# Kernel tuning notes

Hardware: AMD Instinct MI355X
Metric: run time of the kernel (lower is better)

Reference implementation:

```python
import jax, jax.numpy as jnp
from jax import lax
import numpy as np

# dims (match init_kwargs config)
B, L, D = 32, 512, 32          # batch, seq_len, input_dim
H = 256                         # hidden_dim
E = 8                           # num_experts
PLEN, O = 96, 32                # pred_len, output_dim
LAT = 256                       # flow latent_dim
PD, NPROT = 64, 16              # prototype_dim, num_prototypes


def setup_inputs() -> dict:
    key = jax.random.key(0)
    ks = iter(jax.random.split(key, 40))
    def n(shape, scale=0.02):
        return (jax.random.normal(next(ks), shape, jnp.float32) * scale)
    inp = {
        'x': jax.random.normal(next(ks), (B, L, D), jnp.float32),
        # prototypes + projector (metric gating / diversity)
        'prototypes': n((NPROT, PD), 0.5),
        'Wp': n((PD, PD)), 'bp': jnp.zeros((PD,), jnp.float32),
        # expert_feature_extractor: Linear(7D->H), ReLU, Linear(H->PD), LayerNorm(PD)
        'Wf1': n((7 * D, H)), 'bf1': jnp.zeros((H,), jnp.float32),
        'Wf2': n((H, PD)), 'bf2': jnp.zeros((PD,), jnp.float32),
        'ln_g': jnp.ones((PD,), jnp.float32), 'ln_b': jnp.zeros((PD,), jnp.float32),
        # flow encoder (latent mapping of flattened window) + gating head
        'W1': n((L * D, H)), 'b1': jnp.zeros((H,), jnp.float32),
        'W2': n((H, LAT)), 'b2': jnp.zeros((LAT,), jnp.float32),
        'Wg': n((LAT, E)), 'bg': jnp.zeros((E,), jnp.float32),
        'log_temp': jnp.zeros((), jnp.float32),
        # stacked FFT+Mamba expert params (leading axis = expert)
        'Win': n((E, D, H)), 'b_in': jnp.zeros((E, H), jnp.float32),
        'Wfft': n((E, H, H)), 'b_fft': jnp.zeros((E, H), jnp.float32),
        'a_logit': n((E, H), 1.0),
        'Whead': n((E, H, PLEN * O)), 'b_head': jnp.zeros((E, PLEN * O), jnp.float32),
    }
    return inp


def _expert_features(x, Wf1, bf1, Wf2, bf2, ln_g, ln_b):
    # faithful to compute_expert_features: 7 per-channel stats -> MLP -> LayerNorm
    Lf = jnp.float32(x.shape[1])
    x_mean = x.mean(axis=1)
    x_std = x.std(axis=1, ddof=1)             # torch unbiased std
    x_min = x.min(axis=1)
    x_max = x.max(axis=1)
    x_diff_mean = jnp.diff(x, axis=1).mean(axis=1)
    x_trend = (x[:, -1, :] - x[:, 0, :]) / Lf
    x_fft_mag = jnp.abs(jnp.fft.fft(x, axis=1)).mean(axis=1)
    cf = jnp.concatenate([x_mean, x_std, x_min, x_max, x_diff_mean, x_trend, x_fft_mag], axis=1)
    h = jax.nn.relu(cf @ Wf1 + bf1)
    ef = h @ Wf2 + bf2
    mu = ef.mean(axis=-1, keepdims=True)
    var = ef.var(axis=-1, keepdims=True)
    return (ef - mu) / jnp.sqrt(var + 1e-5) * ln_g + ln_b


def reference(x, prototypes, Wp, bp, Wf1, bf1, Wf2, bf2, ln_g, ln_b,
              W1, b1, W2, b2, Wg, bg, log_temp,
              Win, b_in, Wfft, b_fft, a_logit, Whead, b_head):
    b, l, d = x.shape
    # --- metric-based gating ---
    ef = _expert_features(x, Wf1, bf1, Wf2, bf2, ln_g, ln_b)           # [B,PD]
    latent = jax.nn.relu(x.reshape(b, -1) @ W1 + b1) @ W2 + b2          # flow latent [B,LAT]
    lg = latent @ Wg + bg                                               # [B,E]
    proj = ef @ Wp + bp                                                 # prototype_projector
    d2 = ((proj[:, None, :] - prototypes[None, :, :]) ** 2).sum(-1)     # [B,NPROT]
    d2_per_expert = d2.reshape(b, E, NPROT // E).min(axis=-1)           # min dist to each expert's prototypes
    temp = jnp.clip(jnp.exp(log_temp), 0.1, 10.0)
    w = jax.nn.softmax((lg - d2_per_expert) / temp, axis=-1)            # [B,E]

    # --- FFT + Mamba-style experts (vmapped over stacked expert params) ---
    def expert(Win_e, b_in_e, Wfft_e, b_fft_e, a_logit_e, Whead_e, b_head_e):
        h = jnp.einsum('bld,dh->blh', x, Win_e) + b_in_e                # [B,L,H]
        f = jnp.einsum('blh,hk->blk', jnp.abs(jnp.fft.fft(h, axis=1)), Wfft_e) + b_fft_e
        u = jax.nn.relu(h + f)
        a = jax.nn.sigmoid(a_logit_e)                                   # per-channel decay
        def step(s, ut):
            s = a * s + (1.0 - a) * ut
            return s, None
        s_last, _ = lax.scan(step, jnp.zeros((b, H), x.dtype), jnp.swapaxes(u, 0, 1))
        return (s_last @ Whead_e + b_head_e).reshape(b, PLEN, O)

    outs = jax.vmap(expert)(Win, b_in, Wfft, b_fft, a_logit, Whead, b_head)  # [E,B,PLEN,O]
    y = jnp.einsum('be,ebpo->bpo', w, outs)
    return y
```

## Files before the change

kernel.cpp:

```cpp
#include <hip/hip_runtime.h>
#include <hip/hip_bf16.h>


typedef __hip_bfloat16 bf16;
typedef unsigned short u16;
typedef __attribute__((ext_vector_type(8))) short s8v;
typedef __attribute__((ext_vector_type(4))) float f4v;

#define MFMA_BF16(a,b,c) __builtin_amdgcn_mfma_f32_16x16x32_bf16(a,b,c,0,0,0)

#if __has_builtin(__builtin_amdgcn_sqrtf)
#define FSQRT(x) __builtin_amdgcn_sqrtf(x)
#else
#define FSQRT(x) sqrtf(x)
#endif
#if __has_builtin(__builtin_amdgcn_exp2f)
#define FEXP2(x) __builtin_amdgcn_exp2f(x)
#else
#define FEXP2(x) exp2f(x)
#endif
#if __has_builtin(__builtin_amdgcn_logf)
#define FLOG2(x) __builtin_amdgcn_logf(x)
#else
#define FLOG2(x) log2f(x)
#endif

#define GWF1 0
#define GW2  57344
#define GWF2 122880
#define GWP  139264
#define GPROT 143360
#define GWG  144384

__device__ __forceinline__ float bf2f(u16 u){
  union{ unsigned u32; float f; } w; w.u32 = ((unsigned)u) << 16; return w.f;
}
__device__ __forceinline__ u16 f2bf(float f){
  bf16 h = __float2bfloat16(f);
  union{ bf16 b; u16 u; } w; w.b = h; return w.u;
}
__device__ __forceinline__ u16 f2bf_fast(float f){
  union{ float f; unsigned u; } v; v.f = f;
  unsigned r = v.u + 0x7FFFu + ((v.u >> 16) & 1u);
  return (u16)(r >> 16);
}
__device__ __forceinline__ float ldg_(const void* p, long long i, bool bf){
  float r;
  if(bf) r = bf2f(((const u16*)p)[i]);
  else   r = ((const float*)p)[i];
  return r;
}
__device__ __forceinline__ bool bfflag(const void* ln_g){
  return ((const u16*)ln_g)[0] == 0x3F80;
}

__global__ __launch_bounds__(256) void ks1(const void* __restrict__ ln_g,
    const void* __restrict__ x,
    const void* __restrict__ Win, const void* __restrict__ Wfft,
    const void* __restrict__ W1, const void* __restrict__ Whead,
    const void* __restrict__ Wf1, const void* __restrict__ W2,
    const void* __restrict__ Wf2, const void* __restrict__ Wp,
    const void* __restrict__ prot, const void* __restrict__ Wg,
    u16* __restrict__ xbf,
    u16* __restrict__ WinTg, u16* __restrict__ WfftTg,
    u16* __restrict__ W1Tg, u16* __restrict__ WheadTg,
    u16* __restrict__ gw,
    u16* __restrict__ Xr, u16* __restrict__ Xi, float* __restrict__ cf){
  const bool bf = bfflag(ln_g);
  __shared__ float xs[512], re[512], im[512];
  __shared__ float twr[256], twi[256];
  __shared__ float r0s[4], r1s[4], r2s[4], r3s[4];
  __shared__ u16 tile[64][72];
  int BX = blockIdx.x, t = threadIdx.x;

  if(BX < 1024){
    int b = BX >> 5, d = BX & 31;
    {
      float rev = -(float)t * (1.f/512.f);
#if __has_builtin(__builtin_amdgcn_cosf) && __has_builtin(__builtin_amdgcn_sinf)
      twr[t] = __builtin_amdgcn_cosf(rev);
      twi[t] = __builtin_amdgcn_sinf(rev);
#else
      float ang = rev * 6.283185307179586f;
      twr[t] = cosf(ang); twi[t] = sinf(ang);
#endif
    }
    for(int i=t;i<512;i+=256){
      float v = ldg_(x, (long long)(b*512+i)*32 + d, bf);
      xs[i] = v;
      re[__brev((unsigned)i) >> 23] = v;
      im[i] = 0.f;
    }
    __syncthreads();
    float s=0.f, s2=0.f, mn=3.0e38f, mx=-3.0e38f;
    for(int i=t;i<512;i+=256){ float v=xs[i]; s+=v; s2+=v*v; mn=fminf(mn,v); mx=fmaxf(mx,v); }
    #pragma unroll
    for(int o=32;o>0;o>>=1){
      s  += __shfl_down(s,o);  s2 += __shfl_down(s2,o);
      mn = fminf(mn,__shfl_down(mn,o)); mx = fmaxf(mx,__shfl_down(mx,o));
    }
    int wv = t>>6, ln = t&63;
    if(ln==0){ r0s[wv]=s; r1s[wv]=s2; r2s[wv]=mn; r3s[wv]=mx; }
    __syncthreads();
    if(t==0){
      float S =r0s[0]+r0s[1]+r0s[2]+r0s[3];
      float S2=r1s[0]+r1s[1]+r1s[2]+r1s[3];
      float MN=fminf(fminf(r2s[0],r2s[1]),fminf(r2s[2],r2s[3]));
      float MX=fmaxf(fmaxf(r3s[0],r3s[1]),fmaxf(r3s[2],r3s[3]));
      float mean = S*(1.f/512.f);
      float var  = (S2 - S*S*(1.f/512.f))*(1.f/511.f);
      float* c = cf + b*224;
      c[d]      = mean;
      c[32+d]   = sqrtf(fmaxf(var,0.f));
      c[64+d]   = MN;
      c[96+d]   = MX;
      float dv = xs[511]-xs[0];
      c[128+d]  = dv*(1.f/511.f);
      c[160+d]  = dv*(1.f/512.f);
    }
    for(int st=1; st<=9; ++st){
      __syncthreads();
      int m = 1<<st, half = m>>1;
      int grp = t >> (st-1);
      int k   = t & (half-1);
      int i1 = grp*m + k, i2 = i1 + half;
      int ti_ = k << (9-st);
      float cs = twr[ti_], sn = twi[ti_];
      float ar=re[i1], ai=im[i1], br=re[i2], bi=im[i2];
      float tr = cs*br - sn*bi;
      float ti = cs*bi + sn*br;
      re[i1]=ar+tr; im[i1]=ai+ti;
      re[i2]=ar-tr; im[i2]=ai-ti;
    }
    __syncthreads();
    float ms=0.f;
    for(int i=t;i<512;i+=256){
      float rr=re[i], ii=im[i];
      long long o = (long long)(b*512+i)*32 + d;
      Xr[o]=f2bf(rr); Xi[o]=f2bf(ii);
      ms += FSQRT(rr*rr+ii*ii);
    }
    #pragma unroll
    for(int o=32;o>0;o>>=1) ms += __shfl_down(ms,o);
    if(ln==0) r0s[wv]=ms;
    __syncthreads();
    if(t==0) cf[b*224 + 192 + d] = (r0s[0]+r0s[1]+r0s[2]+r0s[3])*(1.f/512.f);
    return;
  }
  if(BX < 4111){
    int bx = BX - 1024;
    if(bx < 256){
      int i = bx*256 + t;
      int e = i >> 13, r = i & 8191;
      int c = r >> 5, d = r & 31;
      WinTg[i] = f2bf(ldg_(Win, (long long)e*8192 + d*256 + c, bf));
      return;
    }
    if(bx < 384){
      int idx = bx - 256;
      int e = idx >> 4, tl = idx & 15, kb = tl >> 2, cb = tl & 3;
      if(bf){
        for(int q=0;q<16;q++){
          int G = q*256 + t; int ki = G >> 6, ci = G & 63;
          tile[ci][ki] = ((const u16*)Wfft)[(long long)e*65536 + (long long)(kb*64+ki)*256 + cb*64+ci];
        }
      } else {
        for(int q=0;q<16;q++){
          int G = q*256 + t; int ki = G >> 6, ci = G & 63;
          tile[ci][ki] = f2bf(((const float*)Wfft)[(long long)e*65536 + (long long)(kb*64+ki)*256 + cb*64+ci]);
        }
      }
      __syncthreads();
      for(int q=0;q<16;q++){
        int G = q*256 + t; int ci = G >> 6, ki = G & 63;
        WfftTg[(long long)e*65536 + (long long)(cb*64+ci)*256 + kb*64+ki] = tile[ci][ki];
      }
      return;
    }
    if(bx < 1408){
      int idx = bx - 384;
      int kb = idx & 255, nb = idx >> 8;
      if(bf){
        for(int q=0;q<16;q++){
          int G = q*256 + t; int ki = G >> 6, ni = G & 63;
          tile[ni][ki] = ((const u16*)W1)[(long long)(kb*64+ki)*256 + nb*64+ni];
        }
      } else {
        for(int q=0;q<16;q++){
          int G = q*256 + t; int ki = G >> 6, ni = G & 63;
          tile[ni][ki] = f2bf(((const float*)W1)[(long long)(kb*64+ki)*256 + nb*64+ni]);
        }
      }
      __syncthreads();
      for(int q=0;q<16;q++){
        int G = q*256 + t; int ni = G >> 6, ki = G & 63;
        W1Tg[(long long)(nb*64+ni)*16384 + kb*64+ki] = tile[ni][ki];
      }
      return;
    }
    if(bx < 2944){
      int idx = bx - 1408;
      int e = idx / 192, rem = idx % 192;
      int kb = rem / 48, nb = rem % 48;
      if(bf){
        for(int q=0;q<16;q++){
          int G = q*256 + t; int ki = G >> 6, ni = G & 63;
          tile[ni][ki] = ((const u16*)Whead)[(long long)e*786432 + (long long)(kb*64+ki)*3072 + nb*64+ni];
        }
      } else {
        for(int q=0;q<16;q++){
          int G = q*256 + t; int ki = G >> 6, ni = G & 63;
          tile[ni][ki] = f2bf(((const float*)Whead)[(long long)e*786432 + (long long)(kb*64+ki)*3072 + nb*64+ni]);
        }
      }
      __syncthreads();
      for(int q=0;q<16;q++){
        int G = q*256 + t; int ni = G >> 6, ki = G & 63;
        WheadTg[(long long)e*786432 + (long long)(nb*64+ni)*256 + kb*64+ki] = tile[ni][ki];
      }
      return;
    }
    {
      int c = bx - 2944;
      const void* src; int dstbase, blkoff;
      if(c < 56)      { src=Wf1;  dstbase=GWF1;  blkoff=c; }
      else if(c <120) { src=W2;   dstbase=GW2;   blkoff=c-56; }
      else if(c <136) { src=Wf2;  dstbase=GWF2;  blkoff=c-120; }
      else if(c <140) { src=Wp;   dstbase=GWP;   blkoff=c-136; }
      else if(c <141) { src=prot; dstbase=GPROT; blkoff=0; }
      else            { src=Wg;   dstbase=GWG;   blkoff=c-141; }
      int i = blkoff*1024 + t*4;
      if(bf){
        ushort4 v = *(const ushort4*)((const u16*)src + i);
        *(ushort4*)(gw + dstbase + i) = v;
      } else {
        float4 f = *(const float4*)((const float*)src + i);
        ushort4 v; v.x=f2bf(f.x); v.y=f2bf(f.y); v.z=f2bf(f.z); v.w=f2bf(f.w);
        *(ushort4*)(gw + dstbase + i) = v;
      }
    }
    return;
  }
  {
    int i = ((BX-4111)*256 + t)*4;
    if(bf){
      ushort4 v = *(const ushort4*)((const u16*)x + i);
      *(ushort4*)(xbf+i) = v;
    } else {
      float4 f = *(const float4*)((const float*)x + i);
      ushort4 v; v.x=f2bf(f.x); v.y=f2bf(f.y); v.z=f2bf(f.z); v.w=f2bf(f.w);
      *(ushort4*)(xbf+i) = v;
    }
  }
}

__global__ __launch_bounds__(256) void ks2(const void* __restrict__ ln_g,
    const u16* __restrict__ xbf, const u16* __restrict__ Xr, const u16* __restrict__ Xi,
    const u16* __restrict__ WinTg, const u16* __restrict__ W1Tg,
    const u16* __restrict__ gw, const float* __restrict__ cf,
    const void* __restrict__ bf1, const void* __restrict__ b_in,
    const void* __restrict__ b_fft, const void* __restrict__ a_logit,
    const void* __restrict__ Win, const void* __restrict__ Wfft,
    float* __restrict__ psum, u16* __restrict__ hmagG,
    float* __restrict__ h1f, float* __restrict__ contrib){
  const bool bf = bfflag(ln_g);
  int BX = blockIdx.x, t = threadIdx.x;
  int w = t >> 6, lane = t & 63, quad = lane >> 4, l15 = lane & 15;
  const f4v zf = (f4v){0.f,0.f,0.f,0.f};
  __shared__ float binS[256];
  __shared__ float cfs[224];
  __shared__ float hm[256];
  __shared__ float xr6[32], xi6[32], x6[32];

  if(BX < 64){
    int kb = BX;
    f4v acc[2][4];
    #pragma unroll
    for(int mt=0;mt<2;mt++)
      #pragma unroll
      for(int nt=0;nt<4;nt++) acc[mt][nt] = zf;
    #pragma unroll
    for(int ks=0;ks<8;ks++){
      long long k = kb*256 + ks*32 + quad*8;
      s8v aF[2], bF[4];
      #pragma unroll
      for(int mt=0;mt<2;mt++)
        aF[mt] = *(const s8v*)(xbf + (long long)(mt*16 + l15)*16384 + k);
      #pragma unroll
      for(int nt=0;nt<4;nt++)
        bF[nt] = *(const s8v*)(W1Tg + (long long)(w*64 + nt*16 + l15)*16384 + k);
      #pragma unroll
      for(int mt=0;mt<2;mt++)
        #pragma unroll
        for(int nt=0;nt<4;nt++)
          acc[mt][nt] = MFMA_BF16(aF[mt], bF[nt], acc[mt][nt]);
    }
    float* po = psum + (long long)kb*8192;
    #pragma unroll
    for(int mt=0;mt<2;mt++)
      #pragma unroll
      for(int nt=0;nt<4;nt++)
        #pragma unroll
        for(int r=0;r<4;r++)
          po[(mt*16 + quad*4 + r)*256 + w*64 + nt*16 + l15] = acc[mt][nt][r];
    return;
  }
  if(BX < 1088){
    int bx = BX - 64;
    int e = bx >> 7, inner = bx & 127;
    int b = inner >> 2, half = (inner >> 1) & 1, kh = inner & 1;
    int row0 = b*512 + half*128;
    binS[t] = ldg_(b_in, e*256+t, bf);
    s8v xrF[2], xiF[2];
    #pragma unroll
    for(int nt=0;nt<2;nt++){
      long long row = row0 + w*32 + nt*16 + l15;
      xrF[nt] = *(const s8v*)(Xr + row*32 + quad*8);
      xiF[nt] = *(const s8v*)(Xi + row*32 + quad*8);
    }
    __syncthreads();
    u16* Ho = hmagG + (long long)((e<<6)|(b<<1)|half)*32768;
    #pragma unroll
    for(int kcl=0;kcl<2;kcl++){
      int k0 = (kh*2+kcl)*64;
      #pragma unroll
      for(int ct=0;ct<4;ct++){
        s8v wfr = *(const s8v*)(WinTg + ((long long)e*256 + k0 + ct*16 + l15)*32 + quad*8);
        #pragma unroll
        for(int nt=0;nt<2;nt++){
          f4v hr = MFMA_BF16(wfr, xrF[nt], zf);
          f4v hi = MFMA_BF16(wfr, xiF[nt], zf);
          int rowg = row0 + w*32 + nt*16 + l15;
          bool bin0 = ((rowg & 511) == 0);
          ushort4 pk;
          int cb4 = k0 + ct*16 + quad*4;
          float h0 = hr[0] + (bin0 ? 512.f*binS[cb4+0] : 0.f);
          float h1 = hr[1] + (bin0 ? 512.f*binS[cb4+1] : 0.f);
          float h2 = hr[2] + (bin0 ? 512.f*binS[cb4+2] : 0.f);
          float h3 = hr[3] + (bin0 ? 512.f*binS[cb4+3] : 0.f);
          pk.x = f2bf_fast(FSQRT(h0*h0 + hi[0]*hi[0]));
          pk.y = f2bf_fast(FSQRT(h1*h1 + hi[1]*hi[1]));
          pk.z = f2bf_fast(FSQRT(h2*h2 + hi[2]*hi[2]));
          pk.w = f2bf_fast(FSQRT(h3*h3 + hi[3]*hi[3]));
          *(ushort4*)&Ho[(w*32 + nt*16 + l15)*256 + cb4] = pk;
        }
      }
    }
    return;
  }
  if(BX < 1120){
    int b = BX - 1088;
    if(t < 224) cfs[t] = cf[(long long)b*224 + t];
    __syncthreads();
    float a1 = ldg_(bf1, t, bf);
    const u16* Wp_ = gw + GWF1 + t;
    #pragma unroll 16
    for(int k=0;k<224;k++) a1 += cfs[k]*bf2f(Wp_[k*256]);
    h1f[b*256+t] = fmaxf(a1, 0.f);
    return;
  }
  {
    int bx = BX - 1120;
    int e = bx >> 5, b = bx & 31, j = t;
    if(j < 32){
      long long o = ((long long)(b*512 + 256))*32 + j;
      xr6[j] = bf2f(Xr[o]);
      xi6[j] = bf2f(Xi[o]);
      x6[j]  = bf2f(xbf[o]);
    }
    __syncthreads();
    float sr=0.f, si=0.f, hx=0.f;
    if(bf){
      const u16* Wn = (const u16*)Win + (long long)e*8192 + j;
      #pragma unroll 8
      for(int d=0; d<32; d++){
        float wv = bf2f(Wn[d*256]);
        sr += xr6[d]*wv; si += xi6[d]*wv; hx += x6[d]*wv;
      }
    } else {
      const float* Wn = (const float*)Win + (long long)e*8192 + j;
      #pragma unroll 8
      for(int d=0; d<32; d++){
        float wv = Wn[d*256];
        sr += xr6[d]*wv; si += xi6[d]*wv; hx += x6[d]*wv;
      }
    }
    hm[j] = FSQRT(sr*sr + si*si);
    __syncthreads();
    float f = 0.f;
    if(bf){
      const u16* Wf = (const u16*)Wfft + (long long)e*65536 + j;
      #pragma unroll 8
      for(int k=0;k<256;k++) f += hm[k]*bf2f(Wf[(long long)k*256]);
    } else {
      const float* Wf = (const float*)Wfft + (long long)e*65536 + j;
      #pragma unroll 8
      for(int k=0;k<256;k++) f += hm[k]*Wf[(long long)k*256];
    }
    float a = 1.f/(1.f+__expf(-ldg_(a_logit, e*256+j, bf)));
    a = fminf(fmaxf(a, 1e-12f), 0.99999988f);
    float l2a = FLOG2(a);
    float u = fmaxf(hx + f + ldg_(b_in,e*256+j,bf) + ldg_(b_fft,e*256+j,bf), 0.f);
    contrib[(e*32+b)*256 + j] = u * FEXP2(l2a * 255.f);
  }
}

__global__ __launch_bounds__(256) void ks3(const void* __restrict__ ln_g,
    const float* __restrict__ psum, const float* __restrict__ h1f,
    const u16* __restrict__ gw,
    const void* __restrict__ b1, const void* __restrict__ bf2,
    const void* __restrict__ ln_b, const void* __restrict__ bp,
    const void* __restrict__ b2, const void* __restrict__ bg,
    const void* __restrict__ log_temp,
    const u16* __restrict__ xbf, const u16* __restrict__ hmagG,
    const u16* __restrict__ WinTg, const u16* __restrict__ WfftTg,
    const void* __restrict__ b_in, const void* __restrict__ b_fft,
    const void* __restrict__ a_logit,
    float* __restrict__ wgt, float* __restrict__ sp){
  const bool bf = bfflag(ln_g);
  int BX = blockIdx.x, t = threadIdx.x;
  __shared__ __align__(16) u16 BsT[128][72];
  __shared__ float biasS[128], l2aS[128], aS[128];
  __shared__ float hsL[256], h1L[256], latL[256], efL[64], prL[64];
  __shared__ float red[4][64];
  __shared__ float d2part[16][16], d2s[16], lgpart[32][8];

  if(BX < 32){
    int b = BX;
    {
      float s0=0.f, s1=0.f, s2=0.f, s3=0.f;
      #pragma unroll
      for(int kb=0;kb<64;kb+=4){
        s0 += psum[(long long)(kb+0)*8192 + b*256 + t];
        s1 += psum[(long long)(kb+1)*8192 + b*256 + t];
        s2 += psum[(long long)(kb+2)*8192 + b*256 + t];
        s3 += psum[(long long)(kb+3)*8192 + b*256 + t];
      }
      hsL[t] = fmaxf((s0+s1)+(s2+s3) + ldg_(b1,t,bf), 0.f);
    }
    h1L[t] = h1f[b*256+t];
    __syncthreads();
    {
      float a = ldg_(b2, t, bf);
      const u16* W2p = gw + GW2 + t;
      #pragma unroll 16
      for(int k=0;k<256;k++) a += hsL[k]*bf2f(W2p[k*256]);
      latL[t] = a;
    }
    {
      int p = t>>6, j = t&63;
      float acc = 0.f;
      const u16* Wf2p = gw + GWF2 + p*64*64 + j;
      #pragma unroll 16
      for(int i=0;i<64;i++) acc += h1L[p*64+i]*bf2f(Wf2p[i*64]);
      red[p][j] = acc;
    }
    __syncthreads();
    if(t < 64){
      float a2 = red[0][t]+red[1][t]+red[2][t]+red[3][t] + ldg_(bf2,t,bf);
      float sm=a2, sq=a2*a2;
      #pragma unroll
      for(int o=32;o>0;o>>=1){ sm += __shfl_xor(sm,o); sq += __shfl_xor(sq,o); }
      float mu  = sm*(1.f/64.f);
      float var = sq*(1.f/64.f) - mu*mu;
      efL[t] = (a2-mu)*rsqrtf(fmaxf(var,0.f)+1e-5f)*ldg_(ln_g,t,bf) + ldg_(ln_b,t,bf);
      float p_acc = ldg_(bp, t, bf);
      const u16* Wpp = gw + GWP + t;
      #pragma unroll 16
      for(int k=0;k<64;k++) p_acc += efL[k]*bf2f(Wpp[k*64]);
      prL[t] = p_acc;
    }
    {
      int part = t>>3, e = t&7;
      float gp = 0.f;
      const u16* Wgp = gw + GWG + e;
      #pragma unroll
      for(int i=0;i<8;i++){
        int k = part*8 + i;
        gp += latL[k]*bf2f(Wgp[k*8]);
      }
      lgpart[part][e] = gp;
    }
    __syncthreads();
    {
      int p = t>>4, q4 = t&15;
      float dd = 0.f;
      #pragma unroll
      for(int i=0;i<4;i++){
        int d = q4*4 + i;
        float df = prL[d] - bf2f(gw[GPROT + p*64 + d]);
        dd += df*df;
      }
      d2part[p][q4] = dd;
    }
    __syncthreads();
    if(t < 16){
      float s = 0.f;
      #pragma unroll
      for(int i=0;i<16;i++) s += d2part[t][i];
      d2s[t] = s;
    }
    __syncthreads();
    if(t < 8){
      float g = ldg_(bg, t, bf);
      #pragma unroll
      for(int p=0;p<32;p++) g += lgpart[p][t];
      float d2pe = fminf(d2s[2*t], d2s[2*t+1]);
      float temp = fminf(fmaxf(__expf(ldg_(log_temp,0,bf)), 0.1f), 10.f);
      float v = (g - d2pe) / temp;
      float m = v;
      m = fmaxf(m, __shfl_xor(m,1));
      m = fmaxf(m, __shfl_xor(m,2));
      m = fmaxf(m, __shfl_xor(m,4));
      float ex = __expf(v-m);
      float sum = ex;
      sum += __shfl_xor(sum,1);
      sum += __shfl_xor(sum,2);
      sum += __shfl_xor(sum,4);
      wgt[b*8+t] = ex/sum;
    }
    return;
  }
  {
    int bx = BX - 32;
    int e = bx >> 7, inner = bx & 127;
    int b = inner >> 2, half = (inner >> 1) & 1, cb = inner & 1;
    int row0 = b*512 + half*128;
    int col0 = cb*128;
    int w = t >> 6, lane = t & 63, quad = lane >> 4, l15 = lane & 15;

    if(t < 128){
      int c = col0 + t;
      biasS[t] = ldg_(b_in, e*256+c, bf) + ldg_(b_fft, e*256+c, bf);
      float a = 1.f/(1.f+__expf(-ldg_(a_logit, e*256+c, bf)));
      a = fminf(fmaxf(a, 1e-12f), 0.99999988f);
      aS[t] = a;
      l2aS[t] = FLOG2(a);
    }
    const u16* Ab = hmagG + (long long)((e<<6)|(b<<1)|half)*32768;
    const f4v zf = (f4v){0.f,0.f,0.f,0.f};
    f4v acc[2][8];
    #pragma unroll
    for(int mt=0;mt<2;mt++)
      #pragma unroll
      for(int nt=0;nt<8;nt++) acc[mt][nt] = zf;

    for(int kc=0;kc<4;kc++){
      int k0 = kc*64;
      __syncthreads();
      #pragma unroll
      for(int q=0;q<4;q++){
        int G = q*256 + t;
        int c = G >> 3, k8 = (G & 7)*8;
        *(s8v*)&BsT[c][k8] = *(const s8v*)(WfftTg + ((long long)e*256 + col0 + c)*256 + k0 + k8);
      }
      __syncthreads();
      #pragma unroll
      for(int ks=0;ks<2;ks++){
        int kb = ks*32 + quad*8;
        s8v aF0 = *(const s8v*)(Ab + (w*32 + l15)*256 + k0 + kb);
        s8v aF1 = *(const s8v*)(Ab + (w*32 + 16 + l15)*256 + k0 + kb);
        #pragma unroll
        for(int nt=0;nt<8;nt++){
          s8v bF = *(const s8v*)&BsT[nt*16 + l15][kb];
          acc[0][nt] = MFMA_BF16(aF0, bF, acc[0][nt]);
          acc[1][nt] = MFMA_BF16(aF1, bF, acc[1][nt]);
        }
      }
    }
    s8v xF[2], xFm[2];
    #pragma unroll
    for(int mt=0;mt<2;mt++){
      long long rowO = (long long)row0 + w*32 + mt*16 + l15;
      xF[mt] = *(const s8v*)(xbf + rowO*32 + quad*8);
      int lin = half*128 + w*32 + mt*16 + l15;
      int lm  = (512 - lin) & 511;
      xFm[mt] = *(const s8v*)(xbf + ((long long)b*512 + lm)*32 + quad*8);
    }
    int l0base = half*128 + w*32 + quad*4;
    float mz = (l0base == 0) ? 0.f : 1.f;
    const f4v zf2 = (f4v){0.f,0.f,0.f,0.f};
    float part[8];
    #pragma unroll
    for(int nt=0;nt<8;nt++){
      s8v wfh = *(const s8v*)(WinTg + ((long long)e*256 + col0 + nt*16 + l15)*32 + quad*8);
      f4v hv0 = MFMA_BF16(xF[0],  wfh, zf2);
      f4v hv1 = MFMA_BF16(xF[1],  wfh, zf2);
      f4v hm0 = MFMA_BF16(xFm[0], wfh, zf2);
      f4v hm1 = MFMA_BF16(xFm[1], wfh, zf2);
      int cl = nt*16 + l15;
      float l2a = l2aS[cl], bias = biasS[cl], av = aS[cl];
      float inv_a = FEXP2(-l2a);
      float cO0 = FEXP2(l2a * (float)(511 - l0base));
      float cO1 = FEXP2(l2a * (float)(495 - l0base));
      float cM0 = FEXP2(l2a * (float)(l0base - 1));
      float cM1 = FEXP2(l2a * (float)(l0base + 15));
      float sum = 0.f;
      #pragma unroll
      for(int r=0;r<4;r++){
        float u0 = fmaxf(acc[0][nt][r] + hv0[r] + bias, 0.f);
        sum += u0 * cO0;
        float u1 = fmaxf(acc[1][nt][r] + hv1[r] + bias, 0.f);
        sum += u1 * cO1;
        float m0 = fmaxf(acc[0][nt][r] + hm0[r] + bias, 0.f);
        float w0 = m0 * cM0;
        if(r == 0) w0 *= mz;
        sum += w0;
        float m1 = fmaxf(acc[1][nt][r] + hm1[r] + bias, 0.f);
        sum += m1 * cM1;
        cO0 *= inv_a; cO1 *= inv_a; cM0 *= av; cM1 *= av;
      }
      part[nt] = sum;
    }
    __syncthreads();
    float (*redS)[132] = (float(*)[132])BsT;
    #pragma unroll
    for(int nt=0;nt<8;nt++)
      redS[w*4 + quad][nt*16 + l15] = part[nt];
    __syncthreads();
    if(t < 128){
      float tot = 0.f;
      #pragma unroll
      for(int i=0;i<16;i++) tot += redS[i][t];
      sp[e*16384 + (b*2 + half)*256 + col0 + t] = tot;
    }
  }
}

__global__ __launch_bounds__(256) void k67(const void* __restrict__ ln_g,
    const float* __restrict__ sp, const float* __restrict__ contrib,
    const float* __restrict__ wgt, const void* __restrict__ a_logit,
    const u16* __restrict__ WheadTg, const void* __restrict__ b_head,
    void* __restrict__ out){
  const bool bf = bfflag(ln_g);
  int nb = blockIdx.x, t = threadIdx.x;
  int w = t >> 6, lane = t & 63, quad = lane >> 4, l15 = lane & 15;
  __shared__ __align__(16) u16 ssS[32][264];
  __shared__ float omaS[2048];
  __shared__ float wgtS[256];

  wgtS[t] = wgt[t];
  #pragma unroll
  for(int q=0;q<8;q++){
    int idx = q*256 + t;
    float a = 1.f/(1.f+__expf(-ldg_(a_logit, idx, bf)));
    a = fminf(fmaxf(a, 1e-12f), 0.99999988f);
    omaS[idx] = 1.f - a;
  }
  const f4v zf = (f4v){0.f,0.f,0.f,0.f};
  f4v acc[2][2];
  #pragma unroll
  for(int mt=0;mt<2;mt++)
    #pragma unroll
    for(int nt=0;nt<2;nt++) acc[mt][nt] = zf;

  for(int e=0;e<8;e++){
    __syncthreads();
    {
      float oma = omaS[e*256 + t];
      const float* sp0 = sp + e*16384 + t;
      const float* cb  = contrib + e*8192 + t;
      #pragma unroll
      for(int q=0;q<32;q++){
        float v = oma*(sp0[q*512] + sp0[q*512+256] + cb[q*256]);
        ssS[q][t] = f2bf(v);
      }
    }
    __syncthreads();
    f4v tmp[2][2];
    #pragma unroll
    for(int mt=0;mt<2;mt++)
      #pragma unroll
      for(int nt=0;nt<2;nt++) tmp[mt][nt] = zf;
    #pragma unroll
    for(int ks=0;ks<8;ks++){
      int k = ks*32 + quad*8;
      s8v aF0 = *(const s8v*)&ssS[l15][k];
      s8v aF1 = *(const s8v*)&ssS[16 + l15][k];
      s8v bF[2];
      #pragma unroll
      for(int nt=0;nt<2;nt++)
        bF[nt] = *(const s8v*)(WheadTg + ((long long)e*3072 + nb*128 + w*32 + nt*16 + l15)*256 + k);
      tmp[0][0] = MFMA_BF16(aF0, bF[0], tmp[0][0]);
      tmp[0][1] = MFMA_BF16(aF0, bF[1], tmp[0][1]);
      tmp[1][0] = MFMA_BF16(aF1, bF[0], tmp[1][0]);
      tmp[1][1] = MFMA_BF16(aF1, bF[1], tmp[1][1]);
    }
    #pragma unroll
    for(int nt=0;nt<2;nt++){
      int col = nb*128 + w*32 + nt*16 + l15;
      float bh = ldg_(b_head, (long long)e*3072 + col, bf);
      #pragma unroll
      for(int mt=0;mt<2;mt++)
        #pragma unroll
        for(int r=0;r<4;r++){
          int b = mt*16 + quad*4 + r;
          acc[mt][nt][r] += wgtS[b*8+e]*(tmp[mt][nt][r] + bh);
        }
    }
  }
  #pragma unroll
  for(int mt=0;mt<2;mt++)
    #pragma unroll
    for(int nt=0;nt<2;nt++){
      int col = nb*128 + w*32 + nt*16 + l15;
      #pragma unroll
      for(int r=0;r<4;r++){
        int b = mt*16 + quad*4 + r;
        long long i = (long long)b*3072 + col;
        if(bf) ((u16*)out)[i] = f2bf(acc[mt][nt][r]);
        else   ((float*)out)[i] = acc[mt][nt][r];
      }
    }
}

extern "C" void kernel_launch(void* const* d_in, const int* in_sizes, int n_in,
                              void* d_out, int out_size, void* d_ws, size_t ws_size,
                              hipStream_t stream){
  const void* x       = d_in[0];
  const void* prot    = d_in[1];
  const void* Wp      = d_in[2];
  const void* bp      = d_in[3];
  const void* Wf1     = d_in[4];
  const void* bf1     = d_in[5];
  const void* Wf2     = d_in[6];
  const void* bf2     = d_in[7];
  const void* ln_g    = d_in[8];
  const void* ln_b    = d_in[9];
  const void* W1      = d_in[10];
  const void* b1      = d_in[11];
  const void* W2      = d_in[12];
  const void* b2      = d_in[13];
  const void* Wg      = d_in[14];
  const void* bg      = d_in[15];
  const void* log_temp= d_in[16];
  const void* Win     = d_in[17];
  const void* b_in    = d_in[18];
  const void* Wfft    = d_in[19];
  const void* b_fft   = d_in[20];
  const void* a_logit = d_in[21];
  const void* Whead   = d_in[22];
  const void* b_head  = d_in[23];

  float* ws      = (float*)d_ws;
  float* cf      = ws;
  float* wgt     = cf + 7168;
  float* sp      = wgt + 256;
  float* h1f     = sp + 131072;
  float* contrib = sp + 262144;
  float* psum    = sp + 262144 + 786432;
  u16*   Xr      = (u16*)(psum + 524288);
  u16*   Xi      = Xr + 524288;
  u16*   xbf     = Xi + 524288;
  u16*   WinTg   = xbf + 524288;
  u16*   WfftTg  = WinTg + 65536;
  u16*   W1Tg    = WfftTg + 524288;
  u16*   WheadTg = W1Tg + 4194304;
  u16*   ssbf    = WheadTg + 6291456;
  u16*   gw      = ssbf + 65536;
  u16*   hmagG   = gw + 146432;

  ks1 <<<dim3(4623), dim3(256), 0, stream>>>(ln_g, x, Win, Wfft, W1, Whead,
                                             Wf1, W2, Wf2, Wp, prot, Wg,
                                             xbf, WinTg, WfftTg, W1Tg, WheadTg, gw,
                                             Xr, Xi, cf);
  ks2 <<<dim3(1376), dim3(256), 0, stream>>>(ln_g, xbf, Xr, Xi, WinTg, W1Tg,
                                             gw, cf, bf1, b_in, b_fft, a_logit,
                                             Win, Wfft,
                                             psum, hmagG, h1f, contrib);
  ks3 <<<dim3(1056), dim3(256), 0, stream>>>(ln_g, psum, h1f, gw,
                                             b1, bf2, ln_b, bp, b2, bg, log_temp,
                                             xbf, hmagG, WinTg, WfftTg,
                                             b_in, b_fft, a_logit,
                                             wgt, sp);
  k67 <<<dim3(24),   dim3(256), 0, stream>>>(ln_g, sp, contrib, wgt, a_logit,
                                             WheadTg, b_head, d_out);
}
```

Before: 224.6 us.

## Split head GEMM across experts into separate grid and add mixing kernel

The final head kernel, which looped over all eight experts inside only 24 blocks, becomes a 24x8 grid. Each block computes one expert's head GEMM and writes its unmixed result to a workspace buffer. A new elementwise kernel then applies the gating weights and biases across experts to produce the output. The FFT stage also stops storing spectrum bins above the Nyquist index, relying on conjugate symmetry of the real-input FFT, and the workspace layout is compacted. The cost is an extra launch and a round trip through global memory for the per-expert results.

```diff
diff --git a/kernel.cpp b/kernel.cpp
--- a/kernel.cpp
+++ b/kernel.cpp
@@ -136,8 +136,10 @@
     float ms=0.f;
     for(int i=t;i<512;i+=256){
       float rr=re[i], ii=im[i];
-      long long o = (long long)(b*512+i)*32 + d;
-      Xr[o]=f2bf(rr); Xi[o]=f2bf(ii);
+      if(i <= 256){
+        long long o = (long long)(b*512+i)*32 + d;
+        Xr[o]=f2bf(rr); Xi[o]=f2bf(ii);
+      }
       ms += FSQRT(rr*rr+ii*ii);
     }
     #pragma unroll
@@ -627,91 +629,76 @@
   }
 }
 
-__global__ __launch_bounds__(256) void k67(const void* __restrict__ ln_g,
+__global__ __launch_bounds__(256) void k6_mfma(const void* __restrict__ ln_g,
     const float* __restrict__ sp, const float* __restrict__ contrib,
-    const float* __restrict__ wgt, const void* __restrict__ a_logit,
-    const u16* __restrict__ WheadTg, const void* __restrict__ b_head,
-    void* __restrict__ out){
+    const void* __restrict__ a_logit,
+    const u16* __restrict__ WheadTg, float* __restrict__ yaccE){
   const bool bf = bfflag(ln_g);
-  int nb = blockIdx.x, t = threadIdx.x;
+  int nb = blockIdx.x, e = blockIdx.y;
+  int t = threadIdx.x;
   int w = t >> 6, lane = t & 63, quad = lane >> 4, l15 = lane & 15;
   __shared__ __align__(16) u16 ssS[32][264];
-  __shared__ float omaS[2048];
-  __shared__ float wgtS[256];
-
-  wgtS[t] = wgt[t];
-  #pragma unroll
-  for(int q=0;q<8;q++){
-    int idx = q*256 + t;
-    float a = 1.f/(1.f+__expf(-ldg_(a_logit, idx, bf)));
+  {
+    float a = 1.f/(1.f+__expf(-ldg_(a_logit, e*256+t, bf)));
     a = fminf(fmaxf(a, 1e-12f), 0.99999988f);
-    omaS[idx] = 1.f - a;
-  }
+    float oma = 1.f - a;
+    const float* sp0 = sp + e*16384 + t;
+    const float* cb  = contrib + e*8192 + t;
+    #pragma unroll
+    for(int q=0;q<32;q++){
+      float v = oma*(sp0[q*512] + sp0[q*512+256] + cb[q*256]);
+      ssS[q][t] = f2bf(v);
+    }
+  }
+  __syncthreads();
   const f4v zf = (f4v){0.f,0.f,0.f,0.f};
   f4v acc[2][2];
   #pragma unroll
   for(int mt=0;mt<2;mt++)
     #pragma unroll
     for(int nt=0;nt<2;nt++) acc[mt][nt] = zf;
-
-  for(int e=0;e<8;e++){
-    __syncthreads();
-    {
-      float oma = omaS[e*256 + t];
-      const float* sp0 = sp + e*16384 + t;
-      const float* cb  = contrib + e*8192 + t;
-      #pragma unroll
-      for(int q=0;q<32;q++){
-        float v = oma*(sp0[q*512] + sp0[q*512+256] + cb[q*256]);
-        ssS[q][t] = f2bf(v);
-      }
-    }
-    __syncthreads();
-    f4v tmp[2][2];
-    #pragma unroll
-    for(int mt=0;mt<2;mt++)
-      #pragma unroll
-      for(int nt=0;nt<2;nt++) tmp[mt][nt] = zf;
-    #pragma unroll
-    for(int ks=0;ks<8;ks++){
-      int k = ks*32 + quad*8;
-      s8v aF0 = *(const s8v*)&ssS[l15][k];
-      s8v aF1 = *(const s8v*)&ssS[16 + l15][k];
-      s8v bF[2];
-      #pragma unroll
-      for(int nt=0;nt<2;nt++)
-        bF[nt] = *(const s8v*)(WheadTg + ((long long)e*3072 + nb*128 + w*32 + nt*16 + l15)*256 + k);
-      tmp[0][0] = MFMA_BF16(aF0, bF[0], tmp[0][0]);
-      tmp[0][1] = MFMA_BF16(aF0, bF[1], tmp[0][1]);
-      tmp[1][0] = MFMA_BF16(aF1, bF[0], tmp[1][0]);
-      tmp[1][1] = MFMA_BF16(aF1, bF[1], tmp[1][1]);
-    }
+  #pragma unroll
+  for(int ks=0;ks<8;ks++){
+    int k = ks*32 + quad*8;
+    s8v aF0 = *(const s8v*)&ssS[l15][k];
+    s8v aF1 = *(const s8v*)&ssS[16 + l15][k];
+    s8v bF[2];
+    #pragma unroll
+    for(int nt=0;nt<2;nt++)
+      bF[nt] = *(const s8v*)(WheadTg + ((long long)e*3072 + nb*128 + w*32 + nt*16 + l15)*256 + k);
+    acc[0][0] = MFMA_BF16(aF0, bF[0], acc[0][0]);
+    acc[0][1] = MFMA_BF16(aF0, bF[1], acc[0][1]);
+    acc[1][0] = MFMA_BF16(aF1, bF[0], acc[1][0]);
+    acc[1][1] = MFMA_BF16(aF1, bF[1], acc[1][1]);
+  }
+  float* yo = yaccE + (long long)e*98304;
+  #pragma unroll
+  for(int mt=0;mt<2;mt++)
     #pragma unroll
     for(int nt=0;nt<2;nt++){
       int col = nb*128 + w*32 + nt*16 + l15;
-      float bh = ldg_(b_head, (long long)e*3072 + col, bf);
-      #pragma unroll
-      for(int mt=0;mt<2;mt++)
-        #pragma unroll
-        for(int r=0;r<4;r++){
-          int b = mt*16 + quad*4 + r;
-          acc[mt][nt][r] += wgtS[b*8+e]*(tmp[mt][nt][r] + bh);
-        }
-    }
-  }
-  #pragma unroll
-  for(int mt=0;mt<2;mt++)
-    #pragma unroll
-    for(int nt=0;nt<2;nt++){
-      int col = nb*128 + w*32 + nt*16 + l15;
       #pragma unroll
       for(int r=0;r<4;r++){
         int b = mt*16 + quad*4 + r;
-        long long i = (long long)b*3072 + col;
-        if(bf) ((u16*)out)[i] = f2bf(acc[mt][nt][r]);
-        else   ((float*)out)[i] = acc[mt][nt][r];
-      }
-    }
+        yo[b*3072 + col] = acc[mt][nt][r];
+      }
+    }
+}
+
+__global__ void k7_out(const void* __restrict__ ln_g,
+                       const float* __restrict__ yaccE,
+                       const float* __restrict__ wgt,
+                       const void* __restrict__ b_head,
+                       void* __restrict__ out){
+  const bool bf = bfflag(ln_g);
+  int i = blockIdx.x*256 + threadIdx.x;
+  int b = i / 3072, col = i - b*3072;
+  float v = 0.f;
+  #pragma unroll
+  for(int e=0;e<8;e++)
+    v += wgt[b*8+e]*(yaccE[(long long)e*98304 + i] + ldg_(b_head, (long long)e*3072+col, bf));
+  if(bf) ((u16*)out)[i] = f2bf(v);
+  else   ((float*)out)[i] = v;
 }
 
 extern "C" void kernel_launch(void* const* d_in, const int* in_sizes, int n_in,
@@ -747,17 +734,17 @@
   float* wgt     = cf + 7168;
   float* sp      = wgt + 256;
   float* h1f     = sp + 131072;
-  float* contrib = sp + 262144;
-  float* psum    = sp + 262144 + 786432;
-  u16*   Xr      = (u16*)(psum + 524288);
+  float* contrib = h1f + 8192;
+  float* psum    = contrib + 65536;
+  float* yaccE   = psum + 524288;
+  u16*   Xr      = (u16*)(yaccE + 786432);
   u16*   Xi      = Xr + 524288;
   u16*   xbf     = Xi + 524288;
   u16*   WinTg   = xbf + 524288;
   u16*   WfftTg  = WinTg + 65536;
   u16*   W1Tg    = WfftTg + 524288;
   u16*   WheadTg = W1Tg + 4194304;
-  u16*   ssbf    = WheadTg + 6291456;
-  u16*   gw      = ssbf + 65536;
+  u16*   gw      = WheadTg + 6291456;
   u16*   hmagG   = gw + 146432;
 
   ks1 <<<dim3(4623), dim3(256), 0, stream>>>(ln_g, x, Win, Wfft, W1, Whead,
@@ -773,6 +760,7 @@
                                              xbf, hmagG, WinTg, WfftTg,
                                              b_in, b_fft, a_logit,
                                              wgt, sp);
-  k67 <<<dim3(24),   dim3(256), 0, stream>>>(ln_g, sp, contrib, wgt, a_logit,
-                                             WheadTg, b_head, d_out);
-}
+  k6_mfma <<<dim3(24,8), dim3(256), 0, stream>>>(ln_g, sp, contrib, a_logit,
+                                                 WheadTg, yaccE);
+  k7_out  <<<dim3(384),  dim3(256), 0, stream>>>(ln_g, yaccE, wgt, b_head, d_out);
+}
```

After: 196.1 us, median of 2. 12.7% less time.
